# Kernel tuning notes

Measured on AMD Instinct MI355X. Metric: run time of the kernel, lower is better.

## Reference

```python
import jax, jax.numpy as jnp
import numpy as np

T, D, E, K = 16384, 2048, 64, 2
LOAD_BALANCE_SCALE = 0.01
NOISY_STD = 1.0


def setup_inputs() -> dict:
    key = jax.random.key(0)
    k1, k2, k3, k4 = jax.random.split(key, 4)
    x_flat = jax.random.normal(k1, (T, D), dtype=jnp.float32)
    noise = jax.random.normal(k2, (T, E), dtype=jnp.float32)
    # gate_linear: nn.Linear(D, E, bias=False) -> weight [E, D]
    W_gate = jax.random.normal(k3, (E, D), dtype=jnp.float32) * (1.0 / np.sqrt(D))
    # noise_weight initialized to zeros in torch; use small values so the
    # noisy path is exercised numerically.
    noise_weight = jax.random.normal(k4, (E,), dtype=jnp.float32) * 0.01
    return {"x_flat": x_flat, "noise": noise, "W_gate": W_gate,
            "noise_weight": noise_weight, "k": K}


def reference(x_flat, noise, W_gate, noise_weight, k):
    # logits = x @ W^T   [T, E]
    logits = jnp.einsum("td,ed->te", x_flat, W_gate)
    logits_noisy = logits + (noise * NOISY_STD) * noise_weight

    # noisy top-k; softmax over -inf-sparse logits == softmax over the k
    # selected logits scattered into zeros (top-k ids are unique per row).
    top_vals, top_ids = jax.lax.top_k(logits_noisy, k)          # [T, k]
    gates_k = jax.nn.softmax(top_vals, axis=-1)                 # [T, k]
    rows = jnp.arange(x_flat.shape[0])[:, None]
    top_k_gated_weights = jnp.zeros_like(logits_noisy).at[rows, top_ids].set(gates_k)

    # load-balance loss on clean logits
    gate_weights_mean = jax.nn.softmax(logits, axis=-1).mean(axis=0)  # [E]
    uniform = jnp.full_like(gate_weights_mean, 1.0 / gate_weights_mean.shape[0])
    load_balance_loss = jnp.mean((gate_weights_mean - uniform) ** 2) * LOAD_BALANCE_SCALE

    return top_k_gated_weights, top_ids, load_balance_loss
```

## Files before the change

### kernel.cpp

```cpp
#include <hip/hip_runtime.h>
#include <hip/hip_bf16.h>

#define T_TOK 16384
#define D_DIM 2048
#define E_EXP 64
#define TAU   2e-3f

typedef __bf16 bf16x8 __attribute__((ext_vector_type(8)));
typedef float  f32x16 __attribute__((ext_vector_type(16)));
typedef unsigned short ushort_t;

#define WS_WHI  0
#define WS_WLO  (256*1024)
#define WS_SUM  (512*1024)
#define WS_CNT  (512*1024 + 512)
#define WS_FLG  (512*1024 + 1024)

__device__ __forceinline__ unsigned short bf16_rne(float x){
  unsigned int u = __float_as_uint(x);
  return (unsigned short)((u + 0x7FFFu + ((u >> 16) & 1u)) >> 16);
}

__device__ __forceinline__ void ins3(float& v1, int& i1, float& v2, int& i2,
                                     float& v3, int& i3, float v, int i){
  if (v > v1 || (v == v1 && i < i1)) { v3=v2; i3=i2; v2=v1; i2=i1; v1=v; i1=i; }
  else if (v > v2 || (v == v2 && i < i2)) { v3=v2; i3=i2; v2=v; i2=i; }
  else if (v > v3 || (v == v3 && i < i3)) { v3=v; i3=i; }
}

__device__ __forceinline__ void gload16(const void* g, const void* l){
  __builtin_amdgcn_global_load_lds(
      (const __attribute__((address_space(1))) unsigned int*)g,
      (__attribute__((address_space(3))) unsigned int*)l, 16, 0, 0);
}

__global__ void wsplit_kernel(const float* __restrict__ W,
                              ushort_t* __restrict__ whi, ushort_t* __restrict__ wlo,
                              double* __restrict__ ESUM, int* __restrict__ FCNT){
  const int n = blockIdx.x * 256 + threadIdx.x;
  if (blockIdx.x == 0){
    if (threadIdx.x < 64) ESUM[threadIdx.x] = 0.0;
    else if (threadIdx.x == 64) *FCNT = 0;
  }
  const int c = n >> 9, s = n & 511;
  const int grp = s >> 6, l = s & 63;
  const int ks = grp >> 1, nt = grp & 1;
  const int m = l & 31, kg = l >> 5;
  const float* src = W + (size_t)(nt*32 + m)*D_DIM + c*64 + ks*16 + kg*8;
  float4 w0 = *reinterpret_cast<const float4*>(src);
  float4 w1 = *reinterpret_cast<const float4*>(src + 4);
  float f[8] = {w0.x,w0.y,w0.z,w0.w,w1.x,w1.y,w1.z,w1.w};
  unsigned h[8], lo[8];
  #pragma unroll
  for (int i = 0; i < 8; ++i){
    h[i]  = bf16_rne(f[i]);
    lo[i] = bf16_rne(f[i] - __uint_as_float(h[i] << 16));
  }
  uint4 hv = { h[0]|(h[1]<<16),  h[2]|(h[3]<<16),  h[4]|(h[5]<<16),  h[6]|(h[7]<<16) };
  uint4 lv = { lo[0]|(lo[1]<<16), lo[2]|(lo[3]<<16), lo[4]|(lo[5]<<16), lo[6]|(lo[7]<<16) };
  *reinterpret_cast<uint4*>(whi + (size_t)n*8) = hv;
  *reinterpret_cast<uint4*>(wlo + (size_t)n*8) = lv;
}

__launch_bounds__(256, 2)
__global__ void moe_main(const float* __restrict__ X, const float* __restrict__ NZ,
                         const ushort_t* __restrict__ WHI, const ushort_t* __restrict__ WLO,
                         const float* __restrict__ NW, float* __restrict__ OUT,
                         double* __restrict__ ESUM, int* __restrict__ FCNT,
                         int* __restrict__ FLIST)
{
  __shared__ __align__(16) char smem[73728];

  const int tid  = threadIdx.x;
  const int lane = tid & 63;
  const int wv   = tid >> 6;
  const int nt   = wv & 1;
  const int kh   = wv >> 1;
  const int r0   = blockIdx.x << 5;
  const int m    = lane & 31;
  const int kg   = lane >> 5;

  const int ga  = wv*64 + lane;
  const int rA  = ga >> 4, gxp = ga & 15;
  const int gxA = gxp ^ (rA & 15);
  const char* px0 = (const char*)X + ((size_t)(r0 + rA)*D_DIM + gxA*4) * 4;
  const char* px1 = px0 + (size_t)16*D_DIM*4;
  const char* pwh = (const char*)WHI + (size_t)(wv*64 + lane)*16;
  const char* pwl = (const char*)WLO + (size_t)(wv*64 + lane)*16;

  f32x16 acc;
  #pragma unroll
  for (int i = 0; i < 16; ++i) acc[i] = 0.0f;

  #define ISSUE(c, Boff) do{                                                   \
    const size_t xo = (size_t)(c)*256, wo = (size_t)(c)*8192;                  \
    gload16(px0 + xo,        smem + (Boff) +          wv*1024);                \
    gload16(px1 + xo,        smem + (Boff) +       (wv+4)*1024);               \
    gload16(pwh + wo,        smem + (Boff) + 8192  +  wv*1024);                \
    gload16(pwh + wo + 4096, smem + (Boff) + 8192  + (wv+4)*1024);             \
    gload16(pwl + wo,        smem + (Boff) + 16384 +  wv*1024);                \
    gload16(pwl + wo + 4096, smem + (Boff) + 16384 + (wv+4)*1024);             \
  }while(0)

  #define COMPUTE(Boff) do{                                                    \
    const char* Bp = smem + (Boff);                                            \
    _Pragma("unroll")                                                          \
    for (int ks2 = 0; ks2 < 2; ++ks2){                                         \
      const int ks = kh*2 + ks2;                                               \
      float4 fa = *reinterpret_cast<const float4*>(Bp + m*256 + (((ks*4+kg*2  ) ^ (m&15))<<4)); \
      float4 fb = *reinterpret_cast<const float4*>(Bp + m*256 + (((ks*4+kg*2+1) ^ (m&15))<<4)); \
      bf16x8 bh = *reinterpret_cast<const bf16x8*>(Bp + 8192  + ((((ks<<1)|nt)<<10) | (lane<<4))); \
      bf16x8 bl = *reinterpret_cast<const bf16x8*>(Bp + 16384 + ((((ks<<1)|nt)<<10) | (lane<<4))); \
      float fv[8] = {fa.x,fa.y,fa.z,fa.w,fb.x,fb.y,fb.z,fb.w};                 \
      bf16x8 ah, al;                                                           \
      _Pragma("unroll")                                                        \
      for (int ii = 0; ii < 8; ++ii){                                          \
        __bf16 hh = (__bf16)fv[ii];                                            \
        ah[ii] = hh; al[ii] = (__bf16)(fv[ii] - (float)hh);                    \
      }                                                                        \
      acc = __builtin_amdgcn_mfma_f32_32x32x16_bf16(ah, bh, acc, 0, 0, 0);     \
      acc = __builtin_amdgcn_mfma_f32_32x32x16_bf16(ah, bl, acc, 0, 0, 0);     \
      acc = __builtin_amdgcn_mfma_f32_32x32x16_bf16(al, bh, acc, 0, 0, 0);     \
    }                                                                          \
  }while(0)

  #define WAITV(n) do{ asm volatile("s_waitcnt vmcnt(" #n ")" ::: "memory");   \
                       __builtin_amdgcn_sched_barrier(0); }while(0)

  ISSUE(0, 0); ISSUE(1, 24576); ISSUE(2, 49152);

  #pragma unroll 1
  for (int g = 0; g < 10; ++g){
    const int c = g*3;
    WAITV(12); __builtin_amdgcn_s_barrier();
    COMPUTE(0);
    __builtin_amdgcn_s_barrier();
    if (c < 29) ISSUE(c+3, 0);
    WAITV(12); __builtin_amdgcn_s_barrier();
    COMPUTE(24576);
    __builtin_amdgcn_s_barrier();
    if (c+1 < 29) ISSUE(c+4, 24576);
    WAITV(12); __builtin_amdgcn_s_barrier();
    COMPUTE(49152);
    __builtin_amdgcn_s_barrier();
    if (c+2 < 29) ISSUE(c+5, 49152);
  }
  WAITV(6);  __builtin_amdgcn_s_barrier();
  COMPUTE(0);
  __builtin_amdgcn_s_barrier();
  WAITV(0);  __builtin_amdgcn_s_barrier();
  COMPUTE(24576);

  #undef ISSUE
  #undef COMPUTE
  #undef WAITV

  float* lgts = (float*)(smem);
  float* nzs  = (float*)(smem + 8192);
  float* prb  = (float*)(smem + 16384);
  float* nws  = (float*)(smem + 49152);
  const int ex = nt*32 + m;

  if (kh == 0){
    #pragma unroll
    for (int r = 0; r < 16; ++r){
      int rr = (r & 3) + ((r >> 2) << 3) + (kg << 2);
      lgts[rr*64 + ex] = acc[r];
    }
  }
  __syncthreads();
  if (kh == 1){
    #pragma unroll
    for (int r = 0; r < 16; ++r){
      int rr = (r & 3) + ((r >> 2) << 3) + (kg << 2);
      lgts[rr*64 + ex] += acc[r];
    }
  }
  const int sr = tid >> 3, sc = tid & 7;
  {
    *reinterpret_cast<float4*>(&nzs[sr*64 + sc*8]) =
      *reinterpret_cast<const float4*>(NZ + (size_t)(r0 + sr)*E_EXP + sc*8);
    *reinterpret_cast<float4*>(&nzs[sr*64 + sc*8 + 4]) =
      *reinterpret_cast<const float4*>(NZ + (size_t)(r0 + sr)*E_EXP + sc*8 + 4);
  }
  if (tid < 64) nws[tid] = NW[tid];
  __syncthreads();

  {
    const int rrow = (wv << 3) + (lane >> 3);
    const int j    = lane & 7;
    const int trow = r0 + rrow;
    float cl[8];
    float v1 = -INFINITY, v2 = -INFINITY, v3 = -INFINITY;
    int   i1 = 1 << 29,   i2 = 1 << 29,   i3 = 1 << 29;
    #pragma unroll
    for (int mm = 0; mm < 8; ++mm){
      int q = j + (mm << 3);
      float lg = lgts[rrow*64 + q];
      cl[mm] = lg;
      float vn = fmaf(nzs[rrow*64 + q], nws[q], lg);
      ins3(v1,i1,v2,i2,v3,i3, vn, q);
    }
    #pragma unroll
    for (int d = 1; d < 8; d <<= 1){
      float ov1 = __shfl_xor(v1, d, 8), ov2 = __shfl_xor(v2, d, 8), ov3 = __shfl_xor(v3, d, 8);
      int   oi1 = __shfl_xor(i1, d, 8), oi2 = __shfl_xor(i2, d, 8), oi3 = __shfl_xor(i3, d, 8);
      ins3(v1,i1,v2,i2,v3,i3, ov1, oi1);
      ins3(v1,i1,v2,i2,v3,i3, ov2, oi2);
      ins3(v1,i1,v2,i2,v3,i3, ov3, oi3);
    }
    float e1 = expf(v2 - v1);
    float g0 = 1.0f / (1.0f + e1);
    float g1 = e1 * g0;

    float mx = cl[0];
    #pragma unroll
    for (int mm = 1; mm < 8; ++mm) mx = fmaxf(mx, cl[mm]);
    #pragma unroll
    for (int d = 1; d < 8; d <<= 1) mx = fmaxf(mx, __shfl_xor(mx, d, 8));
    float sum = 0.0f, exv[8];
    #pragma unroll
    for (int mm = 0; mm < 8; ++mm){ exv[mm] = expf(cl[mm] - mx); sum += exv[mm]; }
    #pragma unroll
    for (int d = 1; d < 8; d <<= 1) sum += __shfl_xor(sum, d, 8);
    float inv = 1.0f / sum;
    #pragma unroll
    for (int mm = 0; mm < 8; ++mm) prb[rrow*64 + j + (mm << 3)] = exv[mm] * inv;

    if (j == 0){
      OUT[(size_t)T_TOK*E_EXP + (size_t)trow*2]     = (float)i1;
      OUT[(size_t)T_TOK*E_EXP + (size_t)trow*2 + 1] = (float)i2;
      if ((v1 - v2 < TAU) || (v2 - v3 < TAU)){
        int slot = atomicAdd(FCNT, 1);
        FLIST[slot] = trow;
      }
    }
    #pragma unroll
    for (int mm = 0; mm < 8; ++mm){
      int q = j + (mm << 3);
      lgts[rrow*64 + q] = (q == i1) ? g0 : ((q == i2) ? g1 : 0.0f);
    }
  }
  __syncthreads();

  {
    *reinterpret_cast<float4*>(OUT + (size_t)(r0 + sr)*E_EXP + sc*8) =
      *reinterpret_cast<const float4*>(&lgts[sr*64 + sc*8]);
    *reinterpret_cast<float4*>(OUT + (size_t)(r0 + sr)*E_EXP + sc*8 + 4) =
      *reinterpret_cast<const float4*>(&lgts[sr*64 + sc*8 + 4]);
  }
  if (tid < 64){
    float s0 = 0.0f;
    #pragma unroll 8
    for (int rr2 = 0; rr2 < 32; ++rr2) s0 += prb[rr2*64 + tid];
    atomicAdd(&ESUM[tid], (double)s0);
  }
}

__launch_bounds__(256)
__global__ void moe_fixup(const float* __restrict__ X, const float* __restrict__ NZ,
                          const float* __restrict__ WG, const float* __restrict__ NW,
                          float* __restrict__ OUT, const int* __restrict__ FCNT,
                          const int* __restrict__ FLIST)
{
  __shared__ __align__(16) float xl[2048];
  __shared__ double lz[64];
  __shared__ int   si1, si2;
  __shared__ float sg0, sg1;
  const int n    = *FCNT;
  const int lane = threadIdx.x & 63;
  const int wv   = threadIdx.x >> 6;
  for (int idx = blockIdx.x; idx < n; idx += gridDim.x){
    const int t = FLIST[idx];
    {
      int off = threadIdx.x * 8;
      *reinterpret_cast<float4*>(xl + off) =
        *reinterpret_cast<const float4*>(X + (size_t)t*D_DIM + off);
      *reinterpret_cast<float4*>(xl + off + 4) =
        *reinterpret_cast<const float4*>(X + (size_t)t*D_DIM + off + 4);
    }
    __syncthreads();
    for (int s = 0; s < 16; ++s){
      const int e = wv*16 + s;
      const float* wr = WG + (size_t)e*D_DIM;
      double acc = 0.0;
      #pragma unroll
      for (int it = 0; it < 8; ++it){
        float4 w4 = *reinterpret_cast<const float4*>(wr + it*256 + lane*4);
        float4 x4 = *reinterpret_cast<const float4*>(xl + it*256 + lane*4);
        acc += (double)x4.x * (double)w4.x;
        acc += (double)x4.y * (double)w4.y;
        acc += (double)x4.z * (double)w4.z;
        acc += (double)x4.w * (double)w4.w;
      }
      #pragma unroll
      for (int off = 1; off < 64; off <<= 1) acc += __shfl_xor(acc, off, 64);
      if (lane == 0)
        lz[e] = acc + (double)NZ[(size_t)t*E_EXP + e] * (double)NW[e];
    }
    __syncthreads();
    if (threadIdx.x == 0){
      double b1 = -1e300, b2 = -1e300; int j1 = 0, j2 = 0;
      for (int q = 0; q < 64; ++q){
        double v = lz[q];
        if (v > b1){ b2 = b1; j2 = j1; b1 = v; j1 = q; }
        else if (v > b2){ b2 = v; j2 = q; }
      }
      double ee = exp(b2 - b1);
      sg0 = (float)(1.0 / (1.0 + ee));
      sg1 = (float)(ee / (1.0 + ee));
      si1 = j1; si2 = j2;
      OUT[(size_t)T_TOK*E_EXP + (size_t)t*2]     = (float)j1;
      OUT[(size_t)T_TOK*E_EXP + (size_t)t*2 + 1] = (float)j2;
    }
    __syncthreads();
    if (threadIdx.x < 64)
      OUT[(size_t)t*E_EXP + threadIdx.x] = (threadIdx.x == si1) ? sg0 :
                                           ((threadIdx.x == si2) ? sg1 : 0.0f);
    __syncthreads();
  }
}

__global__ void moe_loss(const double* __restrict__ ESUM, float* __restrict__ OUT){
  const int e = threadIdx.x;
  double d = ESUM[e] * (1.0 / T_TOK) - (1.0 / 64.0);
  double sq = d * d;
  #pragma unroll
  for (int off = 1; off < 64; off <<= 1) sq += __shfl_xor(sq, off, 64);
  if (e == 0) OUT[(size_t)T_TOK*E_EXP + T_TOK*2] = (float)(sq * (0.01 / 64.0));
}

extern "C" void kernel_launch(void* const* d_in, const int* in_sizes, int n_in,
                              void* d_out, int out_size, void* d_ws, size_t ws_size,
                              hipStream_t stream)
{
  const float* X  = (const float*)d_in[0];
  const float* NZ = (const float*)d_in[1];
  const float* WG = (const float*)d_in[2];
  const float* NW = (const float*)d_in[3];
  float* OUT = (float*)d_out;
  char*  ws  = (char*)d_ws;
  ushort_t* WHI = (ushort_t*)(ws + WS_WHI);
  ushort_t* WLO = (ushort_t*)(ws + WS_WLO);
  double* ESUM = (double*)(ws + WS_SUM);
  int* FCNT  = (int*)(ws + WS_CNT);
  int* FLIST = (int*)(ws + WS_FLG);

  wsplit_kernel<<<dim3(64), dim3(256), 0, stream>>>(WG, WHI, WLO, ESUM, FCNT);
  moe_main<<<dim3(T_TOK/32), dim3(256), 0, stream>>>(X, NZ, WHI, WLO, NW, OUT, ESUM, FCNT, FLIST);
  moe_fixup<<<dim3(512), dim3(256), 0, stream>>>(X, NZ, WG, NW, OUT, FCNT, FLIST);
  moe_loss<<<dim3(1), dim3(64), 0, stream>>>(ESUM, OUT);
}
```

Measured before the change: 114.4 us.

## Restructure gate GEMM: 8 waves, register-loaded weights, double-buffered X in LDS

```diff
diff --git a/kernel.cpp b/kernel.cpp
--- a/kernel.cpp
+++ b/kernel.cpp
@@ -42,11 +42,12 @@
     if (threadIdx.x < 64) ESUM[threadIdx.x] = 0.0;
     else if (threadIdx.x == 64) *FCNT = 0;
   }
-  const int c = n >> 9, s = n & 511;
-  const int grp = s >> 6, l = s & 63;
-  const int ks = grp >> 1, nt = grp & 1;
-  const int m = l & 31, kg = l >> 5;
-  const float* src = W + (size_t)(nt*32 + m)*D_DIM + c*64 + ks*16 + kg*8;
+  const int lane = n & 63;
+  const int eh   = (n >> 6) & 1;
+  const int t    = (n >> 7) & 7;
+  const int c    = n >> 10;
+  const float* src = W + (size_t)(eh*32 + (lane & 31))*D_DIM
+                       + c*128 + t*16 + (lane >> 5)*8;
   float4 w0 = *reinterpret_cast<const float4*>(src);
   float4 w1 = *reinterpret_cast<const float4*>(src + 4);
   float f[8] = {w0.x,w0.y,w0.z,w0.w,w1.x,w1.y,w1.z,w1.w};
@@ -62,106 +63,120 @@
   *reinterpret_cast<uint4*>(wlo + (size_t)n*8) = lv;
 }
 
-__launch_bounds__(256, 2)
+__launch_bounds__(512, 4)
 __global__ void moe_main(const float* __restrict__ X, const float* __restrict__ NZ,
                          const ushort_t* __restrict__ WHI, const ushort_t* __restrict__ WLO,
                          const float* __restrict__ NW, float* __restrict__ OUT,
                          double* __restrict__ ESUM, int* __restrict__ FCNT,
                          int* __restrict__ FLIST)
 {
-  __shared__ __align__(16) char smem[73728];
+  __shared__ __align__(16) char smem[32768];
 
   const int tid  = threadIdx.x;
   const int lane = tid & 63;
   const int wv   = tid >> 6;
-  const int nt   = wv & 1;
-  const int kh   = wv >> 1;
+  const int eh   = wv & 1;
+  const int ks   = wv >> 1;
   const int r0   = blockIdx.x << 5;
   const int m    = lane & 31;
   const int kg   = lane >> 5;
 
-  const int ga  = wv*64 + lane;
-  const int rA  = ga >> 4, gxp = ga & 15;
-  const int gxA = gxp ^ (rA & 15);
-  const char* px0 = (const char*)X + ((size_t)(r0 + rA)*D_DIM + gxA*4) * 4;
+  const int n0   = wv*64 + lane;
+  const int row0 = n0 >> 5, g0 = n0 & 31;
+  const int gs0  = (g0 & 24) | ((g0 ^ row0) & 7);
+  const char* px0 = (const char*)X + ((size_t)(r0 + row0)*D_DIM + gs0*4) * 4;
   const char* px1 = px0 + (size_t)16*D_DIM*4;
-  const char* pwh = (const char*)WHI + (size_t)(wv*64 + lane)*16;
-  const char* pwl = (const char*)WLO + (size_t)(wv*64 + lane)*16;
+  const char* ldsx0 = smem +        wv*1024;
+  const char* ldsx1 = smem + 8192 + wv*1024;
+
+  const char* pwh = (const char*)WHI + (size_t)(ks*256 + eh*64 + lane)*16;
+  const char* pwl = (const char*)WLO + (size_t)(ks*256 + eh*64 + lane)*16;
+
+  const int gf0 = ks*8 + kg*2;
+  const int gf1 = gf0 + 4;
+  const int offA0 = m*512 + (((gf0  ) & 24) | (((gf0  ) ^ m) & 7))*16;
+  const int offB0 = m*512 + (((gf0+1) & 24) | (((gf0+1) ^ m) & 7))*16;
+  const int offA1 = m*512 + (((gf1  ) & 24) | (((gf1  ) ^ m) & 7))*16;
+  const int offB1 = m*512 + (((gf1+1) & 24) | (((gf1+1) ^ m) & 7))*16;
 
   f32x16 acc;
   #pragma unroll
   for (int i = 0; i < 16; ++i) acc[i] = 0.0f;
 
-  #define ISSUE(c, Boff) do{                                                   \
-    const size_t xo = (size_t)(c)*256, wo = (size_t)(c)*8192;                  \
-    gload16(px0 + xo,        smem + (Boff) +          wv*1024);                \
-    gload16(px1 + xo,        smem + (Boff) +       (wv+4)*1024);               \
-    gload16(pwh + wo,        smem + (Boff) + 8192  +  wv*1024);                \
-    gload16(pwh + wo + 4096, smem + (Boff) + 8192  + (wv+4)*1024);             \
-    gload16(pwl + wo,        smem + (Boff) + 16384 +  wv*1024);                \
-    gload16(pwl + wo + 4096, smem + (Boff) + 16384 + (wv+4)*1024);             \
-  }while(0)
-
-  #define COMPUTE(Boff) do{                                                    \
-    const char* Bp = smem + (Boff);                                            \
+  uint4 whA0, wlA0, whA1, wlA1;
+  uint4 whB0, wlB0, whB1, wlB1;
+
+  #define LOADW(c, H0, L0, H1, L1) do{                                         \
+    H0 = *reinterpret_cast<const uint4*>(pwh + (size_t)(c)*16384);             \
+    L0 = *reinterpret_cast<const uint4*>(pwl + (size_t)(c)*16384);             \
+    H1 = *reinterpret_cast<const uint4*>(pwh + (size_t)(c)*16384 + 2048);      \
+    L1 = *reinterpret_cast<const uint4*>(pwl + (size_t)(c)*16384 + 2048);      \
+  }while(0)
+
+  #define ISSUE(c, BUF, H0, L0, H1, L1) do{                                    \
+    __builtin_amdgcn_sched_barrier(0);                                         \
+    gload16(px0 + (size_t)(c)*512, ldsx0 + (BUF));                             \
+    gload16(px1 + (size_t)(c)*512, ldsx1 + (BUF));                             \
+    LOADW(c, H0, L0, H1, L1);                                                  \
+    __builtin_amdgcn_sched_barrier(0);                                         \
+  }while(0)
+
+  #define CVT8(fa, fb, ah, al) do{                                             \
+    float fv[8] = {fa.x,fa.y,fa.z,fa.w,fb.x,fb.y,fb.z,fb.w};                   \
     _Pragma("unroll")                                                          \
-    for (int ks2 = 0; ks2 < 2; ++ks2){                                         \
-      const int ks = kh*2 + ks2;                                               \
-      float4 fa = *reinterpret_cast<const float4*>(Bp + m*256 + (((ks*4+kg*2  ) ^ (m&15))<<4)); \
-      float4 fb = *reinterpret_cast<const float4*>(Bp + m*256 + (((ks*4+kg*2+1) ^ (m&15))<<4)); \
-      bf16x8 bh = *reinterpret_cast<const bf16x8*>(Bp + 8192  + ((((ks<<1)|nt)<<10) | (lane<<4))); \
-      bf16x8 bl = *reinterpret_cast<const bf16x8*>(Bp + 16384 + ((((ks<<1)|nt)<<10) | (lane<<4))); \
-      float fv[8] = {fa.x,fa.y,fa.z,fa.w,fb.x,fb.y,fb.z,fb.w};                 \
-      bf16x8 ah, al;                                                           \
-      _Pragma("unroll")                                                        \
-      for (int ii = 0; ii < 8; ++ii){                                          \
-        __bf16 hh = (__bf16)fv[ii];                                            \
-        ah[ii] = hh; al[ii] = (__bf16)(fv[ii] - (float)hh);                    \
-      }                                                                        \
-      acc = __builtin_amdgcn_mfma_f32_32x32x16_bf16(ah, bh, acc, 0, 0, 0);     \
-      acc = __builtin_amdgcn_mfma_f32_32x32x16_bf16(ah, bl, acc, 0, 0, 0);     \
-      acc = __builtin_amdgcn_mfma_f32_32x32x16_bf16(al, bh, acc, 0, 0, 0);     \
+    for (int ii = 0; ii < 8; ++ii){                                            \
+      __bf16 hh = (__bf16)fv[ii];                                              \
+      ah[ii] = hh; al[ii] = (__bf16)(fv[ii] - (float)hh);                      \
     }                                                                          \
   }while(0)
 
-  #define WAITV(n) do{ asm volatile("s_waitcnt vmcnt(" #n ")" ::: "memory");   \
-                       __builtin_amdgcn_sched_barrier(0); }while(0)
-
-  ISSUE(0, 0); ISSUE(1, 24576); ISSUE(2, 49152);
+  #define KS2(BUF, OA, OB, WH, WL) do{                                         \
+    float4 fa = *reinterpret_cast<const float4*>(smem + (BUF) + (OA));         \
+    float4 fb = *reinterpret_cast<const float4*>(smem + (BUF) + (OB));         \
+    bf16x8 ah, al;                                                             \
+    CVT8(fa, fb, ah, al);                                                      \
+    bf16x8 bh = __builtin_bit_cast(bf16x8, WH);                                \
+    bf16x8 bl = __builtin_bit_cast(bf16x8, WL);                                \
+    acc = __builtin_amdgcn_mfma_f32_32x32x16_bf16(ah, bh, acc, 0, 0, 0);       \
+    acc = __builtin_amdgcn_mfma_f32_32x32x16_bf16(ah, bl, acc, 0, 0, 0);       \
+    acc = __builtin_amdgcn_mfma_f32_32x32x16_bf16(al, bh, acc, 0, 0, 0);       \
+  }while(0)
+
+  #define PHASE(cc, H0, L0, H1, L1, BUF, WNTOK, DOISS) do{                     \
+    asm volatile("s_waitcnt vmcnt(" WNTOK ")" ::: "memory");                   \
+    __builtin_amdgcn_sched_barrier(0);                                         \
+    __builtin_amdgcn_s_barrier();                                              \
+    KS2(BUF, offA0, offB0, H0, L0);                                            \
+    KS2(BUF, offA1, offB1, H1, L1);                                            \
+    __builtin_amdgcn_s_barrier();                                              \
+    if (DOISS) ISSUE((cc) + 2, BUF, H0, L0, H1, L1);                           \
+  }while(0)
+
+  ISSUE(0, 0,     whA0, wlA0, whA1, wlA1);
+  ISSUE(1, 16384, whB0, wlB0, whB1, wlB1);
 
   #pragma unroll 1
-  for (int g = 0; g < 10; ++g){
-    const int c = g*3;
-    WAITV(12); __builtin_amdgcn_s_barrier();
-    COMPUTE(0);
-    __builtin_amdgcn_s_barrier();
-    if (c < 29) ISSUE(c+3, 0);
-    WAITV(12); __builtin_amdgcn_s_barrier();
-    COMPUTE(24576);
-    __builtin_amdgcn_s_barrier();
-    if (c+1 < 29) ISSUE(c+4, 24576);
-    WAITV(12); __builtin_amdgcn_s_barrier();
-    COMPUTE(49152);
-    __builtin_amdgcn_s_barrier();
-    if (c+2 < 29) ISSUE(c+5, 49152);
-  }
-  WAITV(6);  __builtin_amdgcn_s_barrier();
-  COMPUTE(0);
-  __builtin_amdgcn_s_barrier();
-  WAITV(0);  __builtin_amdgcn_s_barrier();
-  COMPUTE(24576);
-
+  for (int g = 0; g < 7; ++g){
+    PHASE(2*g,     whA0, wlA0, whA1, wlA1, 0,     "6", 1);
+    PHASE(2*g + 1, whB0, wlB0, whB1, wlB1, 16384, "6", 1);
+  }
+  PHASE(14, whA0, wlA0, whA1, wlA1, 0,     "6", 0);
+  PHASE(15, whB0, wlB0, whB1, wlB1, 16384, "0", 0);
+
+  #undef PHASE
+  #undef KS2
+  #undef CVT8
   #undef ISSUE
-  #undef COMPUTE
-  #undef WAITV
+  #undef LOADW
 
   float* lgts = (float*)(smem);
   float* nzs  = (float*)(smem + 8192);
   float* prb  = (float*)(smem + 16384);
-  float* nws  = (float*)(smem + 49152);
-  const int ex = nt*32 + m;
-
-  if (kh == 0){
+  float* nws  = (float*)(smem + 24576);
+  const int ex = eh*32 + m;
+
+  __syncthreads();
+  if (ks == 0){
     #pragma unroll
     for (int r = 0; r < 16; ++r){
       int rr = (r & 3) + ((r >> 2) << 3) + (kg << 2);
@@ -169,24 +184,25 @@
     }
   }
   __syncthreads();
-  if (kh == 1){
-    #pragma unroll
-    for (int r = 0; r < 16; ++r){
-      int rr = (r & 3) + ((r >> 2) << 3) + (kg << 2);
-      lgts[rr*64 + ex] += acc[r];
-    }
-  }
-  const int sr = tid >> 3, sc = tid & 7;
-  {
-    *reinterpret_cast<float4*>(&nzs[sr*64 + sc*8]) =
-      *reinterpret_cast<const float4*>(NZ + (size_t)(r0 + sr)*E_EXP + sc*8);
-    *reinterpret_cast<float4*>(&nzs[sr*64 + sc*8 + 4]) =
-      *reinterpret_cast<const float4*>(NZ + (size_t)(r0 + sr)*E_EXP + sc*8 + 4);
-  }
+  #pragma unroll
+  for (int p = 1; p < 4; ++p){
+    if (ks == p){
+      #pragma unroll
+      for (int r = 0; r < 16; ++r){
+        int rr = (r & 3) + ((r >> 2) << 3) + (kg << 2);
+        lgts[rr*64 + ex] += acc[r];
+      }
+    }
+    __syncthreads();
+  }
+
+  const int sr = tid >> 4, sc = tid & 15;
+  *reinterpret_cast<float4*>(&nzs[sr*64 + sc*4]) =
+    *reinterpret_cast<const float4*>(NZ + (size_t)(r0 + sr)*E_EXP + sc*4);
   if (tid < 64) nws[tid] = NW[tid];
   __syncthreads();
 
-  {
+  if (wv < 4){
     const int rrow = (wv << 3) + (lane >> 3);
     const int j    = lane & 7;
     const int trow = r0 + rrow;
@@ -210,8 +226,8 @@
       ins3(v1,i1,v2,i2,v3,i3, ov3, oi3);
     }
     float e1 = expf(v2 - v1);
-    float g0 = 1.0f / (1.0f + e1);
-    float g1 = e1 * g0;
+    float g0g = 1.0f / (1.0f + e1);
+    float g1g = e1 * g0g;
 
     float mx = cl[0];
     #pragma unroll
@@ -238,17 +254,13 @@
     #pragma unroll
     for (int mm = 0; mm < 8; ++mm){
       int q = j + (mm << 3);
-      lgts[rrow*64 + q] = (q == i1) ? g0 : ((q == i2) ? g1 : 0.0f);
+      lgts[rrow*64 + q] = (q == i1) ? g0g : ((q == i2) ? g1g : 0.0f);
     }
   }
   __syncthreads();
 
-  {
-    *reinterpret_cast<float4*>(OUT + (size_t)(r0 + sr)*E_EXP + sc*8) =
-      *reinterpret_cast<const float4*>(&lgts[sr*64 + sc*8]);
-    *reinterpret_cast<float4*>(OUT + (size_t)(r0 + sr)*E_EXP + sc*8 + 4) =
-      *reinterpret_cast<const float4*>(&lgts[sr*64 + sc*8 + 4]);
-  }
+  *reinterpret_cast<float4*>(OUT + (size_t)(r0 + sr)*E_EXP + sc*4) =
+    *reinterpret_cast<const float4*>(&lgts[sr*64 + sc*4]);
   if (tid < 64){
     float s0 = 0.0f;
     #pragma unroll 8
@@ -347,7 +359,7 @@
   int* FLIST = (int*)(ws + WS_FLG);
 
   wsplit_kernel<<<dim3(64), dim3(256), 0, stream>>>(WG, WHI, WLO, ESUM, FCNT);
-  moe_main<<<dim3(T_TOK/32), dim3(256), 0, stream>>>(X, NZ, WHI, WLO, NW, OUT, ESUM, FCNT, FLIST);
+  moe_main<<<dim3(T_TOK/32), dim3(512), 0, stream>>>(X, NZ, WHI, WLO, NW, OUT, ESUM, FCNT, FLIST);
   moe_fixup<<<dim3(512), dim3(256), 0, stream>>>(X, NZ, WG, NW, OUT, FCNT, FLIST);
   moe_loss<<<dim3(1), dim3(64), 0, stream>>>(ESUM, OUT);
 }
```

New measurement: 113.1 us. About the same (-1.1%).
